# Kernel optimization log

Hardware: AMD Instinct MI355X
Metric: run time of the kernel (lower is better)

The kernel has to match this reference:

```python
import jax, jax.numpy as jnp
import numpy as np

B = 4             # graphs per batch
POS_RANGE = 240.0 # pos lives in [0, 240)^3
VOXELS = (20.0, 30.0, 50.0, 80.0)
NEG = -1e30


def _basis(u):
    # open B-spline basis, degree 1, kernel_size 2, dim 3 -> 8 weights per edge
    cols = []
    for k in range(8):
        w = (u[:, 0] if k & 4 else 1.0 - u[:, 0])
        w = w * (u[:, 1] if k & 2 else 1.0 - u[:, 1])
        w = w * (u[:, 2] if k & 1 else 1.0 - u[:, 2])
        cols.append(w)
    return jnp.stack(cols, axis=1)  # [E, 8]


def _cartesian(pos, src, dst, emask):
    # T.Cartesian(cat=False, norm=True): rel pos scaled into [0,1]
    rel = pos[src] - pos[dst]
    m = jnp.max(jnp.where(emask[:, None], jnp.abs(rel), 0.0))
    return rel / (2.0 * jnp.maximum(m, 1e-9)) + 0.5


def _spline_conv(x, src, dst, pseudo, emask, W, Wr, b, n_nodes):
    # out_i = mean_{j->i} sum_k B_k(u_ij) x_j W_k + x_i Wr + b
    basis = _basis(pseudo) * emask[:, None].astype(x.dtype)  # [E,8]
    xk = jnp.einsum('ni,kio->nko', x, W)                     # [N,8,O]
    msg = basis[:, 0, None] * xk[src, 0]
    for k in range(1, 8):
        msg = msg + basis[:, k, None] * xk[src, k]           # [E,O]
    agg = jax.ops.segment_sum(msg, dst, num_segments=n_nodes)
    deg = jax.ops.segment_sum(emask.astype(x.dtype), dst, num_segments=n_nodes)
    return agg / jnp.maximum(deg, 1.0)[:, None] + x @ Wr + b


def _voxel_ids(pos, batch, vs):
    G = int(np.ceil(POS_RANGE / vs))
    c = jnp.clip(jnp.floor(pos / vs).astype(jnp.int64), 0, G - 1)
    cell = (c[:, 0] * G + c[:, 1]) * G + c[:, 2]
    return batch * (G ** 3) + cell, G ** 3


def _max_pool(x, pos, batch, valid, src, dst, emask, vs):
    # voxel-grid max pooling: nodes become fixed voxel cells (empty cells masked)
    nid, ncells = _voxel_ids(pos, batch, vs)
    n_new = B * ncells
    xm = jnp.where(valid[:, None], x, NEG)
    x_p = jax.ops.segment_max(xm, nid, num_segments=n_new)
    cnt = jax.ops.segment_sum(valid.astype(x.dtype), nid, num_segments=n_new)
    v_new = cnt > 0
    x_p = jnp.where(v_new[:, None], x_p, 0.0)
    pos_p = jax.ops.segment_sum(pos * valid[:, None].astype(pos.dtype), nid, num_segments=n_new)
    pos_p = pos_p / jnp.maximum(cnt, 1.0)[:, None]
    batch_p = jnp.arange(n_new, dtype=jnp.int64) // ncells
    # coarsen edges: remap to cells, drop self loops, coalesce at fixed size
    s2, d2 = nid[src], nid[dst]
    sent = n_new * n_new
    key = jnp.where(emask & (s2 != d2), s2 * n_new + d2, sent)
    uk = jnp.unique(key, size=key.shape[0], fill_value=sent)
    em = uk != sent
    uk = jnp.where(em, uk, 0)
    return x_p, pos_p, batch_p, v_new, uk // n_new, uk % n_new, em


def setup_inputs():
    key = jax.random.key(0)
    ks = jax.random.split(key, 24)
    NP, DEG = 5000, 8
    N = B * NP
    E = N * DEG
    x = jax.random.normal(ks[0], (N, 1), dtype=jnp.float32)
    pos = jax.random.uniform(ks[1], (N, 3), dtype=jnp.float32) * POS_RANGE
    src = jnp.repeat(jnp.arange(N, dtype=jnp.int64), DEG)
    delta = jax.random.randint(ks[2], (E,), 1, 100, dtype=jnp.int64)
    dst = (src // NP) * NP + (src % NP + delta) % NP   # intra-graph edges
    edge_index = jnp.stack([src, dst])
    batch = jnp.arange(N, dtype=jnp.int64) // NP
    sizes = [1, 64, 128, 256, 512]
    params = {}
    for l in range(4):
        ci, co = sizes[l], sizes[l + 1]
        params[f'W{l+1}'] = jax.random.normal(ks[3 + 3 * l], (8, ci, co), dtype=jnp.float32) / np.sqrt(8.0 * ci)
        params[f'Wr{l+1}'] = jax.random.normal(ks[4 + 3 * l], (ci, co), dtype=jnp.float32) / np.sqrt(float(ci))
        params[f'b{l+1}'] = jnp.zeros((co,), dtype=jnp.float32)
    params['fc1_w'] = jax.random.normal(ks[16], (64 * 512, 1024), dtype=jnp.float32) / np.sqrt(64.0 * 512.0)
    params['fc1_b'] = jnp.zeros((1024,), dtype=jnp.float32)
    params['fc2_w'] = jax.random.normal(ks[17], (1024, 1), dtype=jnp.float32) / np.sqrt(1024.0)
    params['fc2_b'] = jnp.zeros((1,), dtype=jnp.float32)
    return dict(x=x, pos=pos, edge_index=edge_index, batch=batch, **params)


def reference(x, pos, edge_index, batch, W1, Wr1, b1, W2, Wr2, b2, W3, Wr3, b3,
              W4, Wr4, b4, fc1_w, fc1_b, fc2_w, fc2_b):
    src, dst = edge_index[0], edge_index[1]
    n_nodes = x.shape[0]
    valid = jnp.ones((n_nodes,), dtype=bool)
    emask = jnp.ones((src.shape[0],), dtype=bool)
    Ws = [(W1, Wr1, b1), (W2, Wr2, b2), (W3, Wr3, b3), (W4, Wr4, b4)]
    for l in range(4):
        pseudo = _cartesian(pos, src, dst, emask)
        W, Wr, b = Ws[l]
        x = jax.nn.elu(_spline_conv(x, src, dst, pseudo, emask, W, Wr, b, n_nodes))
        if l < 3:
            x, pos, batch, valid, src, dst, emask = _max_pool(x, pos, batch, valid, src, dst, emask, VOXELS[l])
            n_nodes = x.shape[0]
    # MaxPoolingX(voxel=80, size=64): ceil(240/80)^3 = 27 <= 64 slots per graph
    nid, ncells = _voxel_ids(pos, batch, VOXELS[3])
    cluster = batch * 64 + (nid % ncells)
    xm = jnp.where(valid[:, None], x, NEG)
    xg = jax.ops.segment_max(xm, cluster, num_segments=B * 64)
    xg = jnp.where(xg <= NEG / 2, 0.0, xg)      # empty slots -> 0 (scatter-max default)
    xg = xg.reshape(B, 64 * 512)
    h = jax.nn.elu(xg @ fc1_w + fc1_b)           # dropout = identity (eval mode)
    return jax.nn.elu(h @ fc2_w + fc2_b)         # [B, 1]
```

## Files before the change

kernel.cpp:

```cpp
#include <hip/hip_runtime.h>

static constexpr int E0 = 160000;
static constexpr int NL0 = 20000;
static constexpr int NL1 = 6912;
static constexpr int NL2 = 2048;
static constexpr int NL3 = 500;

typedef short bf16x8 __attribute__((ext_vector_type(8)));
typedef float f32x4 __attribute__((ext_vector_type(4)));

__device__ __forceinline__ unsigned f2ord(float f) {
  unsigned u = __float_as_uint(f);
  return (u & 0x80000000u) ? ~u : (u | 0x80000000u);
}
__device__ __forceinline__ float ord2f(unsigned u) {
  unsigned v = (u & 0x80000000u) ? (u & 0x7fffffffu) : ~u;
  return __uint_as_float(v);
}
__device__ __forceinline__ float eluf(float x) { return x > 0.f ? x : expm1f(x); }
__device__ __forceinline__ void basis8(float u0, float u1, float u2, float* w) {
  float a0 = 1.f - u0, a1 = 1.f - u1, a2 = 1.f - u2;
  w[0] = a0*a1*a2; w[1] = a0*a1*u2; w[2] = a0*u1*a2; w[3] = a0*u1*u2;
  w[4] = u0*a1*a2; w[5] = u0*a1*u2; w[6] = u0*u1*a2; w[7] = u0*u1*u2;
}
__device__ __forceinline__ unsigned short f2b(float f) {
  unsigned u = __float_as_uint(f);
  return (unsigned short)((u + 0x7fffu + ((u >> 16) & 1u)) >> 16);
}
__device__ __forceinline__ float b2f(unsigned short h) {
  return __uint_as_float(((unsigned)h) << 16);
}
__device__ __forceinline__ int clampi(int v, int lo, int hi) {
  return v < lo ? lo : (v > hi ? hi : v);
}

__device__ __forceinline__ void mfma_tile(const unsigned short* __restrict__ Ah,
    const unsigned short* __restrict__ Al, const unsigned short* __restrict__ Bh,
    const unsigned short* __restrict__ Bl, int M, long K, int m0, int n0,
    int kbeg, int ksl, char* smem, f32x4* acc) {
  auto Ash = (unsigned short (*)[40])(smem);
  auto Asl = (unsigned short (*)[40])(smem + 5120);
  auto Bsh = (unsigned short (*)[40])(smem + 10240);
  auto Bsl = (unsigned short (*)[40])(smem + 15360);
  int t = threadIdx.x;
  int r = t >> 2, sg = (t & 3) * 8;
  int w = t >> 6, lane = t & 63;
  int ar = (w << 4) + (lane & 15), kq = (lane >> 4) << 3;
  for (int kt = 0; kt < ksl; kt += 32) {
    bf16x8 va = {}, vl = {};
    if (m0 + r < M) {
      long ga = (long)(m0 + r) * K + kbeg + kt + sg;
      va = *(const bf16x8*)&Ah[ga];
      vl = *(const bf16x8*)&Al[ga];
    }
    *(bf16x8*)&Ash[r][sg] = va;
    *(bf16x8*)&Asl[r][sg] = vl;
    long gb = (long)(n0 + r) * K + kbeg + kt + sg;
    *(bf16x8*)&Bsh[r][sg] = *(const bf16x8*)&Bh[gb];
    *(bf16x8*)&Bsl[r][sg] = *(const bf16x8*)&Bl[gb];
    __syncthreads();
    bf16x8 ah = *(const bf16x8*)&Ash[ar][kq];
    bf16x8 al = *(const bf16x8*)&Asl[ar][kq];
    #pragma unroll
    for (int nt = 0; nt < 4; nt++) {
      int br = (nt << 4) + (lane & 15);
      bf16x8 bh = *(const bf16x8*)&Bsh[br][kq];
      bf16x8 bl = *(const bf16x8*)&Bsl[br][kq];
      acc[nt] = __builtin_amdgcn_mfma_f32_16x16x32_bf16(al, bh, acc[nt], 0, 0, 0);
      acc[nt] = __builtin_amdgcn_mfma_f32_16x16x32_bf16(ah, bl, acc[nt], 0, 0, 0);
      acc[nt] = __builtin_amdgcn_mfma_f32_16x16x32_bf16(ah, bh, acc[nt], 0, 0, 0);
    }
    __syncthreads();
  }
}

__global__ __launch_bounds__(256)
void k_prep(const int* __restrict__ src0, const int* __restrict__ dst0,
            const float* __restrict__ pos0, const float* __restrict__ x0,
            int* __restrict__ degi, int4* __restrict__ erec0u, float* __restrict__ mbuf,
            const float* __restrict__ W1, const float* __restrict__ Wr1, float* __restrict__ wc1,
            const float* __restrict__ W2, const float* __restrict__ Wr2,
            const float* __restrict__ W3, const float* __restrict__ Wr3,
            const float* __restrict__ W4, const float* __restrict__ Wr4,
            unsigned short* __restrict__ w2h, unsigned short* __restrict__ w2l,
            unsigned short* __restrict__ w3h, unsigned short* __restrict__ w3l,
            unsigned short* __restrict__ w4h, unsigned short* __restrict__ w4l) {
  __shared__ __align__(16) float T[64][65];
  __shared__ float red[4];
  int tid = blockIdx.x * 256 + threadIdx.x, gsz = gridDim.x * 256;
  float v = 0.f;
  for (int e = tid; e < E0; e += gsz) {
    int s = src0[e], d = dst0[e];
    atomicAdd(&degi[d], 1);
    float r0 = pos0[s*3]   - pos0[d*3];
    float r1 = pos0[s*3+1] - pos0[d*3+1];
    float r2 = pos0[s*3+2] - pos0[d*3+2];
    erec0u[e] = make_int4(__float_as_int(x0[s]), __float_as_int(r0),
                          __float_as_int(r1), __float_as_int(r2));
    v = fmaxf(v, fmaxf(fabsf(r0), fmaxf(fabsf(r1), fabsf(r2))));
  }
  #pragma unroll
  for (int off = 32; off; off >>= 1) v = fmaxf(v, __shfl_down(v, off, 64));
  if ((threadIdx.x & 63) == 0) red[threadIdx.x >> 6] = v;
  __syncthreads();
  if (threadIdx.x == 0)
    atomicMax((unsigned*)mbuf,
              __float_as_uint(fmaxf(fmaxf(red[0], red[1]), fmaxf(red[2], red[3]))));
  for (int b = blockIdx.x; b < 378; b += gridDim.x) {
    const float *W, *Wr; unsigned short *oh, *ol; int K, N, kt, nt;
    if (b < 18)      { W = W2; Wr = Wr2; oh = w2h; ol = w2l; K = 576;  N = 128; kt = b / 2; nt = b % 2; }
    else if (b < 90) { int q = b - 18; W = W3; Wr = Wr3; oh = w3h; ol = w3l; K = 1152; N = 256; kt = q / 4; nt = q % 4; }
    else             { int q = b - 90; W = W4; Wr = Wr4; oh = w4h; ol = w4l; K = 2304; N = 512; kt = q / 8; nt = q % 8; }
    int k0 = kt * 64, n0 = nt * 64, KW = K - K / 9;
    __syncthreads();
    for (int i = threadIdx.x; i < 4096; i += 256) {
      int kk = i >> 6, nn = i & 63, k = k0 + kk;
      T[kk][nn] = (k < KW) ? W[(long)k * N + n0 + nn] : Wr[(long)(k - KW) * N + n0 + nn];
    }
    __syncthreads();
    for (int i = threadIdx.x; i < 4096; i += 256) {
      int nn = i >> 6, kk = i & 63;
      float vv = T[kk][nn];
      unsigned short hu = f2b(vv), lu = f2b(vv - b2f(hu));
      long o = (long)(n0 + nn) * K + k0 + kk;
      oh[o] = hu; ol[o] = lu;
    }
  }
  if (blockIdx.x == 0)
    for (int i = threadIdx.x; i < 576; i += 256)
      wc1[i] = (i < 512) ? W1[i] : Wr1[i - 512];
}

__global__ void k_alloc(int* __restrict__ degi, int* __restrict__ rowbeg,
                        int* __restrict__ rowlen, int* __restrict__ cursor,
                        int* __restrict__ ctr, int N) {
  int n = blockIdx.x * 256 + threadIdx.x;
  if (n >= N) return;
  int len = degi[n];
  int st = atomicAdd(ctr, len);
  rowbeg[n] = st; cursor[n] = st; rowlen[n] = len; degi[n] = 0;
}

__global__ void k_scat(const int4* __restrict__ eu, const int* __restrict__ du,
                       const int* __restrict__ ecnt, int ecap,
                       int* __restrict__ cursor, int4* __restrict__ es) {
  int n = ecnt ? *ecnt : ecap;
  for (int e = blockIdx.x * 256 + threadIdx.x; e < n; e += gridDim.x * 256) {
    int p = atomicAdd(&cursor[du[e]], 1);
    es[p] = eu[e];
  }
}

__global__ __launch_bounds__(256)
void k_l1(const float* __restrict__ pos0, const float* __restrict__ x0,
          const int4* __restrict__ erec, const int* __restrict__ rowbeg,
          const int* __restrict__ rowlen, const float* __restrict__ mbuf,
          const float* __restrict__ wc1, const float* __restrict__ b1,
          unsigned* __restrict__ pord1, float* __restrict__ cnt1,
          float* __restrict__ possum1, int* __restrict__ nid) {
  __shared__ float ys9[256][12];
  int t = threadIdx.x;
  int d = blockIdx.x * 256 + t;
  float inv = 0.5f / fmaxf(mbuf[0], 1e-9f);
  if (d < NL0) {
    int beg = rowbeg[d], len = rowlen[d];
    float acc[8] = {};
    for (int j = beg; j < beg + len; j++) {
      int4 rc = erec[j];
      float xv = __int_as_float(rc.x);
      float u0 = __int_as_float(rc.y) * inv + 0.5f;
      float u1 = __int_as_float(rc.z) * inv + 0.5f;
      float u2 = __int_as_float(rc.w) * inv + 0.5f;
      float w[8]; basis8(u0, u1, u2, w);
      #pragma unroll
      for (int k = 0; k < 8; k++) acc[k] += w[k] * xv;
    }
    float sc = 1.f / fmaxf((float)len, 1.f);
    #pragma unroll
    for (int k = 0; k < 8; k++) ys9[t][k] = acc[k] * sc;
    ys9[t][8]  = x0[d];
    ys9[t][9]  = pos0[d*3];
    ys9[t][10] = pos0[d*3+1];
    ys9[t][11] = pos0[d*3+2];
  }
  __syncthreads();
  int lane = t & 63, wv = t >> 6;
  float wcol[9];
  #pragma unroll
  for (int k = 0; k < 8; k++) wcol[k] = wc1[k * 64 + lane];
  wcol[8] = wc1[512 + lane];
  float bb = b1[lane];
  int base = blockIdx.x * 256 + wv * 64;
  for (int i = 0; i < 64; i++) {
    int dd = base + i;
    if (dd >= NL0) break;
    int li = wv * 64 + i;
    float v = bb + ys9[li][8] * wcol[8];
    #pragma unroll
    for (int k = 0; k < 8; k++) v += ys9[li][k] * wcol[k];
    v = eluf(v);
    float pd0 = ys9[li][9], pd1 = ys9[li][10], pd2 = ys9[li][11];
    int c0 = clampi((int)floorf(pd0 / 20.f), 0, 11);
    int c1 = clampi((int)floorf(pd1 / 20.f), 0, 11);
    int c2 = clampi((int)floorf(pd2 / 20.f), 0, 11);
    int id = (dd / 5000) * 1728 + (c0 * 12 + c1) * 12 + c2;
    atomicMax(&pord1[(long)id * 64 + lane], f2ord(v));
    if (lane == 0) {
      nid[dd] = id;
      atomicAdd(&cnt1[id], 1.f);
      atomicAdd(&possum1[id*3],   pd0);
      atomicAdd(&possum1[id*3+1], pd1);
      atomicAdd(&possum1[id*3+2], pd2);
    }
  }
}

__global__ __launch_bounds__(256)
void k_pedge(const int4* __restrict__ erecf, const int* __restrict__ srcf,
             const int* __restrict__ dstf, const int* __restrict__ ecntf, int ecap,
             const int* __restrict__ nid, int Nn, unsigned* __restrict__ bitmap,
             int4* __restrict__ erecu, int* __restrict__ dstu, int* __restrict__ ecntc,
             int* __restrict__ degi, const float* __restrict__ possum,
             const float* __restrict__ cnt, float* __restrict__ mo) {
  __shared__ float red[4];
  int n = ecntf ? *ecntf : ecap;
  float vmax = 0.f;
  for (int e = blockIdx.x * 256 + threadIdx.x; e < n; e += gridDim.x * 256) {
    int sL = erecf ? erecf[e].x : srcf[e];
    int dL = dstf[e];
    int s2 = nid[sL], d2 = nid[dL];
    if (s2 == d2) continue;
    float ics = 1.f / fmaxf(cnt[s2], 1.f), icd = 1.f / fmaxf(cnt[d2], 1.f);
    float r0 = possum[s2*3]   * ics - possum[d2*3]   * icd;
    float r1 = possum[s2*3+1] * ics - possum[d2*3+1] * icd;
    float r2 = possum[s2*3+2] * ics - possum[d2*3+2] * icd;
    vmax = fmaxf(vmax, fmaxf(fabsf(r0), fmaxf(fabsf(r1), fabsf(r2))));
    unsigned key = (unsigned)s2 * (unsigned)Nn + (unsigned)d2;
    unsigned bit = 1u << (key & 31);
    unsigned old = atomicOr(&bitmap[key >> 5], bit);
    if (!(old & bit)) {
      int q = atomicAdd(ecntc, 1);
      erecu[q] = make_int4(s2, __float_as_int(r0), __float_as_int(r1), __float_as_int(r2));
      dstu[q] = d2;
      atomicAdd(&degi[d2], 1);
    }
  }
  #pragma unroll
  for (int off = 32; off; off >>= 1) vmax = fmaxf(vmax, __shfl_down(vmax, off, 64));
  if ((threadIdx.x & 63) == 0) red[threadIdx.x >> 6] = vmax;
  __syncthreads();
  if (threadIdx.x == 0)
    atomicMax((unsigned*)mo,
              __float_as_uint(fmaxf(fmaxf(red[0], red[1]), fmaxf(red[2], red[3]))));
}

__global__ __launch_bounds__(256)
void k_gather(const unsigned* __restrict__ pordc, const int4* __restrict__ erec,
              const int* __restrict__ rowbeg, const int* __restrict__ rowlen,
              const float* __restrict__ mbuf,
              unsigned short* __restrict__ ysh, unsigned short* __restrict__ ysl,
              int N, int Ci, int nchunk) {
  int wid = blockIdx.x * 4 + (threadIdx.x >> 6);
  int lane = threadIdx.x & 63;
  int d = wid / nchunk, ch = wid % nchunk;
  if (d >= N) return;
  int co = ch * 64 + lane;
  float inv = 0.5f / fmaxf(mbuf[0], 1e-9f);
  int beg = rowbeg[d], len = rowlen[d], end = beg + len;
  float acc[8] = {};
  int j = beg;
  for (; j + 1 < end; j += 2) {
    int4 ra = erec[j], rb = erec[j + 1];
    float ua0 = __int_as_float(ra.y) * inv + 0.5f;
    float ua1 = __int_as_float(ra.z) * inv + 0.5f;
    float ua2 = __int_as_float(ra.w) * inv + 0.5f;
    float ub0 = __int_as_float(rb.y) * inv + 0.5f;
    float ub1 = __int_as_float(rb.z) * inv + 0.5f;
    float ub2 = __int_as_float(rb.w) * inv + 0.5f;
    float xa = ord2f(pordc[(long)ra.x * Ci + co]);
    float xb = ord2f(pordc[(long)rb.x * Ci + co]);
    float wa[8], wb[8];
    basis8(ua0, ua1, ua2, wa);
    basis8(ub0, ub1, ub2, wb);
    #pragma unroll
    for (int k = 0; k < 8; k++) acc[k] += wa[k] * xa + wb[k] * xb;
  }
  if (j < end) {
    int4 ra = erec[j];
    float ua0 = __int_as_float(ra.y) * inv + 0.5f;
    float ua1 = __int_as_float(ra.z) * inv + 0.5f;
    float ua2 = __int_as_float(ra.w) * inv + 0.5f;
    float xa = ord2f(pordc[(long)ra.x * Ci + co]);
    float wa[8];
    basis8(ua0, ua1, ua2, wa);
    #pragma unroll
    for (int k = 0; k < 8; k++) acc[k] += wa[k] * xa;
  }
  float sc = 1.f / fmaxf((float)len, 1.f);
  long row = (long)d * 9 * Ci;
  #pragma unroll
  for (int k = 0; k < 8; k++) {
    float v = acc[k] * sc;
    unsigned short hu = f2b(v);
    ysh[row + k * Ci + co] = hu;
    ysl[row + k * Ci + co] = f2b(v - b2f(hu));
  }
  float xd = ord2f(pordc[(long)d * Ci + co]);
  unsigned od = pordc[(long)d * Ci + co];
  xd = (od == 0u) ? 0.f : ord2f(od);
  unsigned short hu = f2b(xd);
  ysh[row + 8 * Ci + co] = hu;
  ysl[row + 8 * Ci + co] = f2b(xd - b2f(hu));
}

__global__ __launch_bounds__(256)
void k_gemmpool(const unsigned short* __restrict__ ysh, const unsigned short* __restrict__ ysl,
                const unsigned short* __restrict__ Bh, const unsigned short* __restrict__ Bl,
                int M, int N, int K, const float* __restrict__ bias,
                const float* __restrict__ possum, const float* __restrict__ cnt,
                int div, float vs, int G, int NC,
                unsigned* __restrict__ pordn, float* __restrict__ cntn,
                float* __restrict__ possumn, int* __restrict__ nid) {
  __shared__ __align__(16) char smem[20480];
  int nbx = N >> 6;
  int bx = blockIdx.x % nbx, by = blockIdx.x / nbx;
  int m0 = by * 64, n0 = bx * 64;
  f32x4 acc[4] = {};
  mfma_tile(ysh, ysl, Bh, Bl, M, K, m0, n0, 0, K, smem, acc);
  int w = threadIdx.x >> 6, lane = threadIdx.x & 63;
  int row0 = m0 + (w << 4) + ((lane >> 4) << 2);
  int colb = n0 + (lane & 15);
  #pragma unroll
  for (int q = 0; q < 4; q++) {
    int gm = row0 + q;
    float c = cnt[gm];
    float ic = 1.f / fmaxf(c, 1.f);
    float p0 = possum[gm*3] * ic, p1 = possum[gm*3+1] * ic, p2 = possum[gm*3+2] * ic;
    int c0 = clampi((int)floorf(p0 / vs), 0, G - 1);
    int c1 = clampi((int)floorf(p1 / vs), 0, G - 1);
    int c2 = clampi((int)floorf(p2 / vs), 0, G - 1);
    int id = (gm / div) * NC + (c0 * G + c1) * G + c2;
    bool vl = c > 0.f;
    if (bx == 0 && (lane & 15) == 0) {
      nid[gm] = id;
      if (vl) {
        atomicAdd(&cntn[id], 1.f);
        atomicAdd(&possumn[id*3],   p0);
        atomicAdd(&possumn[id*3+1], p1);
        atomicAdd(&possumn[id*3+2], p2);
      }
    }
    if (vl) {
      #pragma unroll
      for (int nt = 0; nt < 4; nt++) {
        int col = colb + nt * 16;
        float v = eluf(acc[nt][q] + bias[col]);
        atomicMax(&pordn[(long)id * N + col], f2ord(v));
      }
    }
  }
}

__global__ __launch_bounds__(256)
void k_gemm4(const unsigned short* __restrict__ ysh, const unsigned short* __restrict__ ysl,
             const unsigned short* __restrict__ Bh, const unsigned short* __restrict__ Bl,
             float* __restrict__ Cp) {
  __shared__ __align__(16) char smem[20480];
  int z = blockIdx.x >> 6, rem = blockIdx.x & 63, bx = rem & 7, by = rem >> 3;
  int m0 = by * 64, n0 = bx * 64;
  f32x4 acc[4] = {};
  mfma_tile(ysh, ysl, Bh, Bl, 500, 2304, m0, n0, z * 576, 576, smem, acc);
  float* Co = Cp + (long)z * 256000;
  int w = threadIdx.x >> 6, lane = threadIdx.x & 63;
  int row0 = m0 + (w << 4) + ((lane >> 4) << 2);
  int colb = n0 + (lane & 15);
  #pragma unroll
  for (int nt = 0; nt < 4; nt++)
    #pragma unroll
    for (int q = 0; q < 4; q++) {
      int gm = row0 + q;
      if (gm < 500) Co[(long)gm * 512 + colb + nt * 16] = acc[nt][q];
    }
}

__global__ void k_reduce4(const float* __restrict__ Cp, const float* __restrict__ b4,
                          const float* __restrict__ possum3, const float* __restrict__ cnt3,
                          unsigned* __restrict__ xg) {
  int idx = blockIdx.x * 256 + threadIdx.x;
  if (idx >= 256000) return;
  int n = idx >> 9, o = idx & 511;
  float s = Cp[idx] + Cp[idx + 256000] + Cp[idx + 512000] + Cp[idx + 768000];
  float v = eluf(s + b4[o]);
  float c = cnt3[n];
  if (c <= 0.f) return;
  float ic = 1.f / c;
  float p0 = possum3[n*3] * ic, p1 = possum3[n*3+1] * ic, p2 = possum3[n*3+2] * ic;
  int c0 = clampi((int)floorf(p0 / 80.f), 0, 2);
  int c1 = clampi((int)floorf(p1 / 80.f), 0, 2);
  int c2 = clampi((int)floorf(p2 / 80.f), 0, 2);
  int cl = (n / 125) * 64 + (c0 * 3 + c1) * 3 + c2;
  atomicMax(&xg[(long)cl * 512 + o], f2ord(v));
}

__global__ __launch_bounds__(128)
void k_fc1(const unsigned* __restrict__ xg_ord, const float* __restrict__ w,
           float* __restrict__ h) {
  int cellhalf = blockIdx.x >> 3, jb = blockIdx.x & 7;
  int cell = cellhalf >> 1, half = cellhalf & 1;
  int j = jb * 128 + threadIdx.x;
  __shared__ float xs[4][256];
  for (int q = threadIdx.x; q < 1024; q += 128) {
    int b = q >> 8, ci = q & 255;
    unsigned o = xg_ord[((b * 64 + cell) << 9) + half * 256 + ci];
    xs[b][ci] = (o == 0u) ? 0.f : ord2f(o);
  }
  __syncthreads();
  float a0 = 0, a1 = 0, a2 = 0, a3 = 0;
  int cbase = cell * 512 + half * 256;
  for (int ci = 0; ci < 256; ci++) {
    float ww = w[(long)(cbase + ci) * 1024 + j];
    a0 += xs[0][ci] * ww; a1 += xs[1][ci] * ww;
    a2 += xs[2][ci] * ww; a3 += xs[3][ci] * ww;
  }
  atomicAdd(&h[j], a0);        atomicAdd(&h[1024 + j], a1);
  atomicAdd(&h[2048 + j], a2); atomicAdd(&h[3072 + j], a3);
}

__global__ void k_fc2(const float* __restrict__ h, const float* __restrict__ fb1,
                      const float* __restrict__ w, const float* __restrict__ b,
                      float* __restrict__ out) {
  int bb = blockIdx.x, t = threadIdx.x;
  float a = 0;
  for (int j = t; j < 1024; j += 256) a += eluf(h[bb * 1024 + j] + fb1[j]) * w[j];
  for (int off = 32; off; off >>= 1) a += __shfl_down(a, off, 64);
  __shared__ float red[4];
  int lane = t & 63, wv = t >> 6;
  if (lane == 0) red[wv] = a;
  __syncthreads();
  if (t == 0) out[bb] = eluf(red[0] + red[1] + red[2] + red[3] + b[0]);
}

extern "C" void kernel_launch(void* const* d_in, const int* in_sizes, int n_in,
                              void* d_out, int out_size, void* d_ws, size_t ws_size,
                              hipStream_t stream) {
  const float* x0   = (const float*)d_in[0];
  const float* pos0 = (const float*)d_in[1];
  const int*   ei   = (const int*)d_in[2];
  const float* W1 = (const float*)d_in[4],  *Wr1 = (const float*)d_in[5],  *b1 = (const float*)d_in[6];
  const float* W2 = (const float*)d_in[7],  *Wr2 = (const float*)d_in[8],  *b2 = (const float*)d_in[9];
  const float* W3 = (const float*)d_in[10], *Wr3 = (const float*)d_in[11], *b3 = (const float*)d_in[12];
  const float* W4 = (const float*)d_in[13], *Wr4 = (const float*)d_in[14], *b4 = (const float*)d_in[15];
  const float* fw1 = (const float*)d_in[16], *fb1 = (const float*)d_in[17];
  const float* fw2 = (const float*)d_in[18], *fb2 = (const float*)d_in[19];
  float* out = (float*)d_out;
  const int* src0 = ei;
  const int* dst0 = ei + E0;

  char* ws = (char*)d_ws;
  size_t off = 0;
  auto alloc = [&](size_t bytes) -> void* {
    off = (off + 255) & ~(size_t)255;
    void* q = ws + off; off += bytes; return q;
  };
  int4* erec0u = (int4*)alloc((size_t)E0 * 16);
  int4* erec_s = (int4*)alloc((size_t)E0 * 16);
  int4* eu_a   = (int4*)alloc((size_t)E0 * 16);
  int4* eu_b   = (int4*)alloc((size_t)E0 * 16);
  int* du_a = (int*)alloc(E0 * 4);
  int* du_b = (int*)alloc(E0 * 4);
  int* nid  = (int*)alloc(NL0 * 4);
  int* rowbeg = (int*)alloc(NL0 * 4);
  int* rowlen = (int*)alloc(NL0 * 4);
  int* cursor = (int*)alloc(NL0 * 4);
  unsigned short* ysh = (unsigned short*)alloc((size_t)NL1 * 576 * 2);
  unsigned short* ysl = (unsigned short*)alloc((size_t)NL1 * 576 * 2);
  float* wc1 = (float*)alloc(576 * 4);
  unsigned short* w2h = (unsigned short*)alloc((size_t)576 * 128 * 2);
  unsigned short* w2l = (unsigned short*)alloc((size_t)576 * 128 * 2);
  unsigned short* w3h = (unsigned short*)alloc((size_t)1152 * 256 * 2);
  unsigned short* w3l = (unsigned short*)alloc((size_t)1152 * 256 * 2);
  unsigned short* w4h = (unsigned short*)alloc((size_t)2304 * 512 * 2);
  unsigned short* w4l = (unsigned short*)alloc((size_t)2304 * 512 * 2);
  float* Cp = (float*)alloc((size_t)4 * 256000 * 4);
  char* z0 = (char*)alloc(0);
  unsigned* pord1 = (unsigned*)alloc((size_t)NL1 * 64 * 4);
  unsigned* pord2 = (unsigned*)alloc((size_t)NL2 * 128 * 4);
  unsigned* pord3 = (unsigned*)alloc((size_t)NL3 * 256 * 4);
  unsigned* xg    = (unsigned*)alloc((size_t)4 * 64 * 512 * 4);
  float* cnt1 = (float*)alloc(NL1 * 4);
  float* cnt2 = (float*)alloc(NL2 * 4);
  float* cnt3 = (float*)alloc(NL3 * 4);
  float* possum1 = (float*)alloc(NL1 * 12);
  float* possum2 = (float*)alloc(NL2 * 12);
  float* possum3 = (float*)alloc(NL3 * 12);
  size_t bm1w = ((size_t)NL1 * NL1 + 31) / 32;
  size_t bm2w = ((size_t)NL2 * NL2 + 31) / 32;
  size_t bm3w = ((size_t)NL3 * NL3 + 31) / 32;
  unsigned* bm1 = (unsigned*)alloc(bm1w * 4);
  unsigned* bm2 = (unsigned*)alloc(bm2w * 4);
  unsigned* bm3 = (unsigned*)alloc(bm3w * 4);
  int* degi = (int*)alloc(NL0 * 4);
  float* mbuf = (float*)alloc(64);
  int* ecnt = (int*)(mbuf + 8);
  int* ctr  = (int*)(mbuf + 12);
  float* h = (float*)alloc(4096 * 4);
  char* zend = (char*)alloc(0);
  size_t zbytes = (size_t)(zend - z0);
  (void)ws_size; (void)in_sizes; (void)n_in; (void)out_size;

  auto cdiv = [](long a, long b) { return (int)((a + b - 1) / b); };

  hipMemsetAsync(z0, 0, zbytes, stream);

  k_prep<<<512, 256, 0, stream>>>(src0, dst0, pos0, x0, degi, erec0u, mbuf,
                                  W1, Wr1, wc1, W2, Wr2, W3, Wr3, W4, Wr4,
                                  w2h, w2l, w3h, w3l, w4h, w4l);
  k_alloc<<<cdiv(NL0, 256), 256, 0, stream>>>(degi, rowbeg, rowlen, cursor, ctr + 0, NL0);
  k_scat<<<512, 256, 0, stream>>>(erec0u, dst0, nullptr, E0, cursor, erec_s);
  k_l1<<<cdiv(NL0, 256), 256, 0, stream>>>(pos0, x0, erec_s, rowbeg, rowlen, mbuf,
                                           wc1, b1, pord1, cnt1, possum1, nid);
  k_pedge<<<512, 256, 0, stream>>>(nullptr, src0, dst0, nullptr, E0, nid, NL1, bm1,
                                   eu_a, du_a, ecnt + 0, degi, possum1, cnt1, mbuf + 1);
  k_alloc<<<cdiv(NL1, 256), 256, 0, stream>>>(degi, rowbeg, rowlen, cursor, ctr + 1, NL1);
  k_scat<<<512, 256, 0, stream>>>(eu_a, du_a, ecnt + 0, E0, cursor, erec_s);
  k_gather<<<cdiv(NL1, 4), 256, 0, stream>>>(pord1, erec_s, rowbeg, rowlen, mbuf + 1,
                                             ysh, ysl, NL1, 64, 1);
  k_gemmpool<<<(128 / 64) * (NL1 / 64), 256, 0, stream>>>(
      ysh, ysl, w2h, w2l, NL1, 128, 576, b2, possum1, cnt1,
      1728, 30.f, 8, 512, pord2, cnt2, possum2, nid);
  k_pedge<<<512, 256, 0, stream>>>(eu_a, nullptr, du_a, ecnt + 0, E0, nid, NL2, bm2,
                                   eu_b, du_b, ecnt + 1, degi, possum2, cnt2, mbuf + 2);
  k_alloc<<<cdiv(NL2, 256), 256, 0, stream>>>(degi, rowbeg, rowlen, cursor, ctr + 2, NL2);
  k_scat<<<512, 256, 0, stream>>>(eu_b, du_b, ecnt + 1, E0, cursor, erec_s);
  k_gather<<<cdiv(NL2 * 2, 4), 256, 0, stream>>>(pord2, erec_s, rowbeg, rowlen, mbuf + 2,
                                                 ysh, ysl, NL2, 128, 2);
  k_gemmpool<<<(256 / 64) * (NL2 / 64), 256, 0, stream>>>(
      ysh, ysl, w3h, w3l, NL2, 256, 1152, b3, possum2, cnt2,
      512, 50.f, 5, 125, pord3, cnt3, possum3, nid);
  k_pedge<<<512, 256, 0, stream>>>(eu_b, nullptr, du_b, ecnt + 1, E0, nid, NL3, bm3,
                                   eu_a, du_a, ecnt + 2, degi, possum3, cnt3, mbuf + 3);
  k_alloc<<<cdiv(NL3, 256), 256, 0, stream>>>(degi, rowbeg, rowlen, cursor, ctr + 3, NL3);
  k_scat<<<512, 256, 0, stream>>>(eu_a, du_a, ecnt + 2, E0, cursor, erec_s);
  k_gather<<<cdiv(NL3 * 4, 4), 256, 0, stream>>>(pord3, erec_s, rowbeg, rowlen, mbuf + 3,
                                                 ysh, ysl, NL3, 256, 4);
  k_gemm4<<<256, 256, 0, stream>>>(ysh, ysl, w4h, w4l, Cp);
  k_reduce4<<<cdiv(256000, 256), 256, 0, stream>>>(Cp, b4, possum3, cnt3, xg);
  k_fc1<<<27 * 2 * 8, 128, 0, stream>>>(xg, fw1, h);
  k_fc2<<<4, 256, 0, stream>>>(h, fb1, fw2, fb2, out);
}
```

Before: 439.2 us.

## Split gather edges across waves and aggregate pedge edge-counter atomics per wave

In the edge-coarsening kernel, the per-edge atomicAdd on the global compacted-edge counter is replaced by a wave-level ballot, one atomicAdd by a leader lane, and prefix-popcount slot assignment. The gather kernel is templated on ES, so ES waves share one destination row's edge list. Their partial 8-basis accumulators are combined through shared memory, and later layers launch proportionally more blocks to expose parallelism on high-degree coarse nodes. The inner loop is unrolled by four edges to increase memory-level parallelism, at the cost of extra shared memory, a block barrier and more registers.

New measurement: 413.1 us. 5.9% less time.

```diff
diff --git a/kernel.cpp b/kernel.cpp
--- a/kernel.cpp
+++ b/kernel.cpp
@@ -224,25 +224,42 @@
              const float* __restrict__ cnt, float* __restrict__ mo) {
   __shared__ float red[4];
   int n = ecntf ? *ecntf : ecap;
+  int lane = threadIdx.x & 63;
+  int stride = gridDim.x * 256;
   float vmax = 0.f;
-  for (int e = blockIdx.x * 256 + threadIdx.x; e < n; e += gridDim.x * 256) {
-    int sL = erecf ? erecf[e].x : srcf[e];
-    int dL = dstf[e];
-    int s2 = nid[sL], d2 = nid[dL];
-    if (s2 == d2) continue;
-    float ics = 1.f / fmaxf(cnt[s2], 1.f), icd = 1.f / fmaxf(cnt[d2], 1.f);
-    float r0 = possum[s2*3]   * ics - possum[d2*3]   * icd;
-    float r1 = possum[s2*3+1] * ics - possum[d2*3+1] * icd;
-    float r2 = possum[s2*3+2] * ics - possum[d2*3+2] * icd;
-    vmax = fmaxf(vmax, fmaxf(fabsf(r0), fmaxf(fabsf(r1), fabsf(r2))));
-    unsigned key = (unsigned)s2 * (unsigned)Nn + (unsigned)d2;
-    unsigned bit = 1u << (key & 31);
-    unsigned old = atomicOr(&bitmap[key >> 5], bit);
-    if (!(old & bit)) {
-      int q = atomicAdd(ecntc, 1);
-      erecu[q] = make_int4(s2, __float_as_int(r0), __float_as_int(r1), __float_as_int(r2));
-      dstu[q] = d2;
-      atomicAdd(&degi[d2], 1);
+  for (int base = blockIdx.x * 256; base < n; base += stride) {
+    int e = base + threadIdx.x;
+    bool win = false;
+    int s2 = 0, d2 = 0;
+    float r0 = 0.f, r1 = 0.f, r2 = 0.f;
+    if (e < n) {
+      int sL = erecf ? erecf[e].x : srcf[e];
+      int dL = dstf[e];
+      s2 = nid[sL]; d2 = nid[dL];
+      if (s2 != d2) {
+        float ics = 1.f / fmaxf(cnt[s2], 1.f), icd = 1.f / fmaxf(cnt[d2], 1.f);
+        r0 = possum[s2*3]   * ics - possum[d2*3]   * icd;
+        r1 = possum[s2*3+1] * ics - possum[d2*3+1] * icd;
+        r2 = possum[s2*3+2] * ics - possum[d2*3+2] * icd;
+        vmax = fmaxf(vmax, fmaxf(fabsf(r0), fmaxf(fabsf(r1), fabsf(r2))));
+        unsigned key = (unsigned)s2 * (unsigned)Nn + (unsigned)d2;
+        unsigned bit = 1u << (key & 31);
+        unsigned old = atomicOr(&bitmap[key >> 5], bit);
+        win = !(old & bit);
+      }
+    }
+    unsigned long long mask = __ballot(win);
+    if (mask) {
+      int leader = __ffsll((unsigned long long)mask) - 1;
+      int bq = 0;
+      if (lane == leader) bq = atomicAdd(ecntc, __popcll(mask));
+      bq = __shfl(bq, leader, 64);
+      if (win) {
+        int q = bq + __popcll(mask & ((1ULL << lane) - 1ULL));
+        erecu[q] = make_int4(s2, __float_as_int(r0), __float_as_int(r1), __float_as_int(r2));
+        dstu[q] = d2;
+        atomicAdd(&degi[d2], 1);
+      }
     }
   }
   #pragma unroll
@@ -254,48 +271,66 @@
               __float_as_uint(fmaxf(fmaxf(red[0], red[1]), fmaxf(red[2], red[3]))));
 }
 
+template<int ES>
 __global__ __launch_bounds__(256)
 void k_gather(const unsigned* __restrict__ pordc, const int4* __restrict__ erec,
               const int* __restrict__ rowbeg, const int* __restrict__ rowlen,
               const float* __restrict__ mbuf,
               unsigned short* __restrict__ ysh, unsigned short* __restrict__ ysl,
               int N, int Ci, int nchunk) {
-  int wid = blockIdx.x * 4 + (threadIdx.x >> 6);
-  int lane = threadIdx.x & 63;
-  int d = wid / nchunk, ch = wid % nchunk;
-  if (d >= N) return;
+  __shared__ float comb[4][64][8];
+  int wv = threadIdx.x >> 6, lane = threadIdx.x & 63;
+  int gw = blockIdx.x * 4 + wv;
+  int job = gw / ES, sub = gw % ES;
+  int d = job / nchunk, ch = job % nchunk;
+  bool active = d < N;
+  float inv = 0.5f / fmaxf(mbuf[0], 1e-9f);
   int co = ch * 64 + lane;
-  float inv = 0.5f / fmaxf(mbuf[0], 1e-9f);
-  int beg = rowbeg[d], len = rowlen[d], end = beg + len;
   float acc[8] = {};
-  int j = beg;
-  for (; j + 1 < end; j += 2) {
-    int4 ra = erec[j], rb = erec[j + 1];
-    float ua0 = __int_as_float(ra.y) * inv + 0.5f;
-    float ua1 = __int_as_float(ra.z) * inv + 0.5f;
-    float ua2 = __int_as_float(ra.w) * inv + 0.5f;
-    float ub0 = __int_as_float(rb.y) * inv + 0.5f;
-    float ub1 = __int_as_float(rb.z) * inv + 0.5f;
-    float ub2 = __int_as_float(rb.w) * inv + 0.5f;
-    float xa = ord2f(pordc[(long)ra.x * Ci + co]);
-    float xb = ord2f(pordc[(long)rb.x * Ci + co]);
-    float wa[8], wb[8];
-    basis8(ua0, ua1, ua2, wa);
-    basis8(ub0, ub1, ub2, wb);
+  int beg = 0, len = 0;
+  if (active) {
+    beg = rowbeg[d]; len = rowlen[d];
+    int end = beg + len;
+    int j = beg + sub;
+    for (; j + 3 * ES < end; j += 4 * ES) {
+      int4 ra = erec[j], rb = erec[j + ES], rc = erec[j + 2 * ES], rd = erec[j + 3 * ES];
+      float xa = ord2f(pordc[(long)ra.x * Ci + co]);
+      float xb = ord2f(pordc[(long)rb.x * Ci + co]);
+      float xc = ord2f(pordc[(long)rc.x * Ci + co]);
+      float xd = ord2f(pordc[(long)rd.x * Ci + co]);
+      float wa[8], wb[8], wc[8], wd[8];
+      basis8(__int_as_float(ra.y) * inv + 0.5f, __int_as_float(ra.z) * inv + 0.5f,
+             __int_as_float(ra.w) * inv + 0.5f, wa);
+      basis8(__int_as_float(rb.y) * inv + 0.5f, __int_as_float(rb.z) * inv + 0.5f,
+             __int_as_float(rb.w) * inv + 0.5f, wb);
+      basis8(__int_as_float(rc.y) * inv + 0.5f, __int_as_float(rc.z) * inv + 0.5f,
+             __int_as_float(rc.w) * inv + 0.5f, wc);
+      basis8(__int_as_float(rd.y) * inv + 0.5f, __int_as_float(rd.z) * inv + 0.5f,
+             __int_as_float(rd.w) * inv + 0.5f, wd);
+      #pragma unroll
+      for (int k = 0; k < 8; k++)
+        acc[k] += wa[k] * xa + wb[k] * xb + wc[k] * xc + wd[k] * xd;
+    }
+    for (; j < end; j += ES) {
+      int4 ra = erec[j];
+      float xa = ord2f(pordc[(long)ra.x * Ci + co]);
+      float wa[8];
+      basis8(__int_as_float(ra.y) * inv + 0.5f, __int_as_float(ra.z) * inv + 0.5f,
+             __int_as_float(ra.w) * inv + 0.5f, wa);
+      #pragma unroll
+      for (int k = 0; k < 8; k++) acc[k] += wa[k] * xa;
+    }
+  }
+  if (ES > 1) {
     #pragma unroll
-    for (int k = 0; k < 8; k++) acc[k] += wa[k] * xa + wb[k] * xb;
-  }
-  if (j < end) {
-    int4 ra = erec[j];
-    float ua0 = __int_as_float(ra.y) * inv + 0.5f;
-    float ua1 = __int_as_float(ra.z) * inv + 0.5f;
-    float ua2 = __int_as_float(ra.w) * inv + 0.5f;
-    float xa = ord2f(pordc[(long)ra.x * Ci + co]);
-    float wa[8];
-    basis8(ua0, ua1, ua2, wa);
+    for (int k = 0; k < 8; k++) comb[wv][lane][k] = acc[k];
+    __syncthreads();
+    if (sub != 0 || !active) return;
     #pragma unroll
-    for (int k = 0; k < 8; k++) acc[k] += wa[k] * xa;
-  }
+    for (int s = 1; s < ES; s++)
+      #pragma unroll
+      for (int k = 0; k < 8; k++) acc[k] += comb[wv + s][lane][k];
+  } else if (!active) return;
   float sc = 1.f / fmaxf((float)len, 1.f);
   long row = (long)d * 9 * Ci;
   #pragma unroll
@@ -305,12 +340,11 @@
     ysh[row + k * Ci + co] = hu;
     ysl[row + k * Ci + co] = f2b(v - b2f(hu));
   }
-  float xd = ord2f(pordc[(long)d * Ci + co]);
   unsigned od = pordc[(long)d * Ci + co];
-  xd = (od == 0u) ? 0.f : ord2f(od);
-  unsigned short hu = f2b(xd);
+  float xdv = (od == 0u) ? 0.f : ord2f(od);
+  unsigned short hu = f2b(xdv);
   ysh[row + 8 * Ci + co] = hu;
-  ysl[row + 8 * Ci + co] = f2b(xd - b2f(hu));
+  ysl[row + 8 * Ci + co] = f2b(xdv - b2f(hu));
 }
 
 __global__ __launch_bounds__(256)
@@ -523,8 +557,8 @@
                                    eu_a, du_a, ecnt + 0, degi, possum1, cnt1, mbuf + 1);
   k_alloc<<<cdiv(NL1, 256), 256, 0, stream>>>(degi, rowbeg, rowlen, cursor, ctr + 1, NL1);
   k_scat<<<512, 256, 0, stream>>>(eu_a, du_a, ecnt + 0, E0, cursor, erec_s);
-  k_gather<<<cdiv(NL1, 4), 256, 0, stream>>>(pord1, erec_s, rowbeg, rowlen, mbuf + 1,
-                                             ysh, ysl, NL1, 64, 1);
+  k_gather<1><<<cdiv(NL1, 4), 256, 0, stream>>>(pord1, erec_s, rowbeg, rowlen, mbuf + 1,
+                                                ysh, ysl, NL1, 64, 1);
   k_gemmpool<<<(128 / 64) * (NL1 / 64), 256, 0, stream>>>(
       ysh, ysl, w2h, w2l, NL1, 128, 576, b2, possum1, cnt1,
       1728, 30.f, 8, 512, pord2, cnt2, possum2, nid);
@@ -532,8 +566,8 @@
                                    eu_b, du_b, ecnt + 1, degi, possum2, cnt2, mbuf + 2);
   k_alloc<<<cdiv(NL2, 256), 256, 0, stream>>>(degi, rowbeg, rowlen, cursor, ctr + 2, NL2);
   k_scat<<<512, 256, 0, stream>>>(eu_b, du_b, ecnt + 1, E0, cursor, erec_s);
-  k_gather<<<cdiv(NL2 * 2, 4), 256, 0, stream>>>(pord2, erec_s, rowbeg, rowlen, mbuf + 2,
-                                                 ysh, ysl, NL2, 128, 2);
+  k_gather<2><<<cdiv(NL2 * 2 * 2, 4), 256, 0, stream>>>(pord2, erec_s, rowbeg, rowlen, mbuf + 2,
+                                                        ysh, ysl, NL2, 128, 2);
   k_gemmpool<<<(256 / 64) * (NL2 / 64), 256, 0, stream>>>(
       ysh, ysl, w3h, w3l, NL2, 256, 1152, b3, possum2, cnt2,
       512, 50.f, 5, 125, pord3, cnt3, possum3, nid);
@@ -541,8 +575,8 @@
                                    eu_a, du_a, ecnt + 2, degi, possum3, cnt3, mbuf + 3);
   k_alloc<<<cdiv(NL3, 256), 256, 0, stream>>>(degi, rowbeg, rowlen, cursor, ctr + 3, NL3);
   k_scat<<<512, 256, 0, stream>>>(eu_a, du_a, ecnt + 2, E0, cursor, erec_s);
-  k_gather<<<cdiv(NL3 * 4, 4), 256, 0, stream>>>(pord3, erec_s, rowbeg, rowlen, mbuf + 3,
-                                                 ysh, ysl, NL3, 256, 4);
+  k_gather<4><<<cdiv(NL3 * 4 * 4, 4), 256, 0, stream>>>(pord3, erec_s, rowbeg, rowlen, mbuf + 3,
+                                                        ysh, ysl, NL3, 256, 4);
   k_gemm4<<<256, 256, 0, stream>>>(ysh, ysl, w4h, w4l, Cp);
   k_reduce4<<<cdiv(256000, 256), 256, 0, stream>>>(Cp, b4, possum3, cnt3, xg);
   k_fc1<<<27 * 2 * 8, 128, 0, stream>>>(xg, fw1, h);
```
